# Kernel tuning notes

Hardware: AMD Instinct MI355X
Metric: run time of the kernel (lower is better)

## Reference

```python
import jax, jax.numpy as jnp
import numpy as np

N_NODES = 100_000
N_EDGES = 3_200_000


def setup_inputs() -> dict:
    key = jax.random.key(0)
    k = jax.random.split(key, 7)
    x = jax.random.normal(k[0], (N_NODES, 1), dtype=jnp.float32)
    edge_index = jax.random.randint(k[1], (2, N_EDGES), 0, N_NODES, dtype=jnp.int64)
    edge_weight = jax.random.uniform(k[2], (N_EDGES,), dtype=jnp.float32)
    # GCNConv params (glorot-style scale)
    W1 = jax.random.normal(k[3], (1, 16), dtype=jnp.float32) * 0.5
    b1 = jnp.zeros((16,), dtype=jnp.float32)
    W2 = jax.random.normal(k[4], (16, 2), dtype=jnp.float32) * 0.25
    b2 = jnp.zeros((2,), dtype=jnp.float32)
    return {"x": x, "edge_index": edge_index, "edge_weight": edge_weight,
            "W1": W1, "b1": b1, "W2": W2, "b2": b2}


def reference(x, edge_index, edge_weight, W1, b1, W2, b2):
    N = x.shape[0]
    src, dst = edge_index[0], edge_index[1]
    # GCN normalization with self-loops (fill value 1.0), cached across both layers
    loop = jnp.arange(N, dtype=edge_index.dtype)
    src_f = jnp.concatenate([src, loop])            # [E+N]
    dst_f = jnp.concatenate([dst, loop])            # [E+N]
    w_f = jnp.concatenate([edge_weight, jnp.ones((N,), dtype=edge_weight.dtype)])
    deg = jax.ops.segment_sum(w_f, dst_f, num_segments=N)   # [N]
    dinv = jnp.where(deg > 0, jax.lax.rsqrt(deg), 0.0)
    norm = dinv[src_f] * w_f * dinv[dst_f]          # [E+N]

    def gcn_layer(h, W, b):
        h = h @ W                                   # [N, F_out]
        msg = norm[:, None] * h[src_f]              # gather + weight  [E+N, F_out]
        agg = jax.ops.segment_sum(msg, dst_f, num_segments=N)  # scatter-add [N, F_out]
        return agg + b

    h = jax.nn.relu(gcn_layer(x, W1, b1))
    # F.dropout(training=self.training): identity at inference (reference is eval mode)
    out = gcn_layer(h, W2, b2)
    return jax.nn.log_softmax(out, axis=1)
```

## Files before the change

### kernel.cpp

```cpp
#include <hip/hip_runtime.h>
#include <math.h>


static constexpr int BS        = 512;
static constexpr int CHUNK     = 256;
static constexpr int LOG_CHUNK = 8;
static constexpr int MAXNB     = 512;
static constexpr int EPT_H     = 8192;
static constexpr int EPT_P     = 16384;


__global__ __launch_bounds__(BS) void zero_cnt_kernel(unsigned int* __restrict__ cnt,
                                                      int nb) {
    int t = threadIdx.x;
    if (t < nb) cnt[t] = 0u;
}

__global__ __launch_bounds__(BS) void hist_kernel(const int* __restrict__ dst,
                                                  unsigned int* __restrict__ cnt,
                                                  int E, int nb) {
    __shared__ unsigned int h[MAXNB];
    const int t = threadIdx.x;
    for (int i = t; i < nb; i += BS) h[i] = 0u;
    __syncthreads();
    const int base = blockIdx.x * EPT_H;
    const int nE   = min(EPT_H, E - base);
    for (int k = t; k < nE; k += BS)
        atomicAdd(&h[(unsigned int)dst[base + k] >> LOG_CHUNK], 1u);
    __syncthreads();
    for (int i = t; i < nb; i += BS) {
        unsigned int c = h[i];
        if (c) atomicAdd(&cnt[i], c);
    }
}

__global__ __launch_bounds__(BS) void scan_kernel(const unsigned int* __restrict__ cnt,
                                                  unsigned int* __restrict__ start,
                                                  unsigned int* __restrict__ cursor,
                                                  int nb) {
    __shared__ unsigned int s[MAXNB];
    const int t = threadIdx.x;
    unsigned int c = (t < nb) ? cnt[t] : 0u;
    s[t] = c;
    __syncthreads();
    for (int off = 1; off < MAXNB; off <<= 1) {
        unsigned int v = (t >= off) ? s[t - off] : 0u;
        __syncthreads();
        s[t] += v;
        __syncthreads();
    }
    if (t < nb) { start[t + 1] = s[t]; cursor[t] = s[t] - c; }
    if (t == 0) start[0] = 0u;
}

__global__ __launch_bounds__(BS) void place_kernel(
    const int* __restrict__ src, const int* __restrict__ dst,
    const float* __restrict__ w,
    unsigned int* __restrict__ cursor,
    unsigned long long* __restrict__ payload,
    int E, int nb) {
    __shared__ unsigned int h[MAXNB];
    __shared__ unsigned int lcur[MAXNB];
    const int base = blockIdx.x * EPT_P;
    const int nE   = min(EPT_P, E - base);
    const int t    = threadIdx.x;
    for (int i = t; i < nb; i += BS) h[i] = 0u;
    __syncthreads();
    int dc[EPT_P / BS];
    int cnt_ = 0;
    for (int k = t; k < nE; k += BS) {
        int d = dst[base + k];
        dc[cnt_++] = d;
        atomicAdd(&h[(unsigned int)d >> LOG_CHUNK], 1u);
    }
    __syncthreads();
    for (int i = t; i < nb; i += BS) {
        unsigned int c = h[i];
        lcur[i] = c ? atomicAdd(&cursor[i], c) : 0u;
    }
    __syncthreads();
    cnt_ = 0;
    for (int k = t; k < nE; k += BS) {
        int e = base + k;
        int d = dc[cnt_++];
        int b = (unsigned int)d >> LOG_CHUNK;
        unsigned int slot = atomicAdd(&lcur[b], 1u);
        unsigned long long p =
            ((unsigned long long)__float_as_uint(w[e]) << 32) |
            ((unsigned int)src[e] << LOG_CHUNK) |
            (unsigned int)(d & (CHUNK - 1));
        payload[slot] = p;
    }
}


__global__ __launch_bounds__(BS) void deg_dinv_kernel(
    const unsigned long long* __restrict__ payload,
    const unsigned int* __restrict__ start,
    const float* __restrict__ x,
    float* __restrict__ dinv, float* __restrict__ xd, int N) {
    __shared__ float acc[CHUNK];
    const int b = blockIdx.x, t = threadIdx.x;
    if (t < CHUNK) acc[t] = 0.0f;
    __syncthreads();
    const unsigned int s0 = start[b], s1 = start[b + 1];
    for (unsigned int i = s0 + t; i < s1; i += BS) {
        unsigned long long p = payload[i];
        atomicAdd(&acc[(unsigned int)p & (CHUNK - 1)],
                  __uint_as_float((unsigned int)(p >> 32)));
    }
    __syncthreads();
    int n = b * CHUNK + t;
    if (t < CHUNK && n < N) {
        float d = acc[t] + 1.0f;
        float r = (d > 0.0f) ? rsqrtf(d) : 0.0f;
        dinv[n] = r;
        xd[n]   = r * x[n];
    }
}

__global__ __launch_bounds__(BS) void s_gamma_kernel(
    const unsigned long long* __restrict__ payload,
    const unsigned int* __restrict__ start,
    const float* __restrict__ dinv,
    const float* __restrict__ xd,
    const float* __restrict__ W1,
    const float* __restrict__ b1,
    const float* __restrict__ W2,
    float* __restrict__ gd, int N) {
    __shared__ float acc[CHUNK];
    const int b = blockIdx.x, t = threadIdx.x;
    if (t < CHUNK) acc[t] = 0.0f;
    __syncthreads();
    const unsigned int s0 = start[b], s1 = start[b + 1];
    for (unsigned int i = s0 + t; i < s1; i += BS) {
        unsigned long long p = payload[i];
        float wv = __uint_as_float((unsigned int)(p >> 32));
        unsigned int lo32 = (unsigned int)p;
        atomicAdd(&acc[lo32 & (CHUNK - 1)], wv * xd[lo32 >> LOG_CHUNK]);
    }
    __syncthreads();
    int n = b * CHUNK + t;
    if (t < CHUNK && n < N) {
        float dv = dinv[n];
        float sv = dv * (acc[t] + xd[n]);
        float g = 0.0f;
#pragma unroll
        for (int f = 0; f < 16; ++f) {
            float h = fmaxf(sv * W1[f] + b1[f], 0.0f);
            g += h * (W2[2 * f + 1] - W2[2 * f + 0]);
        }
        gd[n] = dv * g;
    }
}

__global__ __launch_bounds__(BS) void d_out_kernel(
    const unsigned long long* __restrict__ payload,
    const unsigned int* __restrict__ start,
    const float* __restrict__ dinv,
    const float* __restrict__ gd,
    const float* __restrict__ b2,
    float* __restrict__ out, int N) {
    __shared__ float acc[CHUNK];
    const int b = blockIdx.x, t = threadIdx.x;
    if (t < CHUNK) acc[t] = 0.0f;
    __syncthreads();
    const unsigned int s0 = start[b], s1 = start[b + 1];
    for (unsigned int i = s0 + t; i < s1; i += BS) {
        unsigned long long p = payload[i];
        float wv = __uint_as_float((unsigned int)(p >> 32));
        unsigned int lo32 = (unsigned int)p;
        atomicAdd(&acc[lo32 & (CHUNK - 1)], wv * gd[lo32 >> LOG_CHUNK]);
    }
    __syncthreads();
    int n = b * CHUNK + t;
    if (t < CHUNK && n < N) {
        float dv = dinv[n];
        float d = dv * (acc[t] + gd[n]) + (b2[1] - b2[0]);
        float lse = fmaxf(d, 0.0f) + log1pf(expf(-fabsf(d)));
        out[2 * n + 0] = -lse;
        out[2 * n + 1] = d - lse;
    }
}


static constexpr int BLOCK = 256;

__global__ void zero_kernel(float* __restrict__ a, float* __restrict__ b, int n2) {
    int i = blockIdx.x * blockDim.x + threadIdx.x;
    if (i < n2) { a[i] = 0.0f; b[i] = 0.0f; }
}
__global__ void deg_kernel(const int* __restrict__ dst, const float* __restrict__ w,
                           float* __restrict__ deg, int E) {
    int e = blockIdx.x * blockDim.x + threadIdx.x;
    if (e < E) atomicAdd(&deg[dst[e]], w[e]);
}
__global__ void dinv_kernel(float* __restrict__ deg, int N) {
    int n = blockIdx.x * blockDim.x + threadIdx.x;
    if (n < N) {
        float d = deg[n] + 1.0f;
        deg[n] = (d > 0.0f) ? rsqrtf(d) : 0.0f;
    }
}
__global__ void s_kernel(const int* __restrict__ src, const int* __restrict__ dst,
                         const float* __restrict__ w, const float* __restrict__ dinv,
                         const float* __restrict__ x, float* __restrict__ s, int E) {
    int e = blockIdx.x * blockDim.x + threadIdx.x;
    if (e < E) {
        int si = src[e], di = dst[e];
        atomicAdd(&s[di], dinv[si] * w[e] * dinv[di] * x[si]);
    }
}
__global__ void g_kernel(const float* __restrict__ s, const float* __restrict__ dinv,
                         const float* __restrict__ x, const float* __restrict__ W1,
                         const float* __restrict__ b1, const float* __restrict__ W2,
                         float2* __restrict__ g, int N) {
    int n = blockIdx.x * blockDim.x + threadIdx.x;
    if (n < N) {
        float dv = dinv[n];
        float sv = s[n] + dv * dv * x[n];
        float g0 = 0.0f, g1 = 0.0f;
#pragma unroll
        for (int f = 0; f < 16; ++f) {
            float h = fmaxf(sv * W1[f] + b1[f], 0.0f);
            g0 += h * W2[2 * f + 0];
            g1 += h * W2[2 * f + 1];
        }
        g[n] = make_float2(g0, g1);
    }
}
__global__ void agg2_kernel(const int* __restrict__ src, const int* __restrict__ dst,
                            const float* __restrict__ w, const float* __restrict__ dinv,
                            const float2* __restrict__ g, float* __restrict__ agg, int E) {
    int e = blockIdx.x * blockDim.x + threadIdx.x;
    if (e < E) {
        int si = src[e], di = dst[e];
        float norm = dinv[si] * w[e] * dinv[di];
        float2 gv = g[si];
        atomicAdd(&agg[2 * di + 0], norm * gv.x);
        atomicAdd(&agg[2 * di + 1], norm * gv.y);
    }
}
__global__ void out_kernel(float* __restrict__ out, const float* __restrict__ dinv,
                           const float2* __restrict__ g, const float* __restrict__ b2, int N) {
    int n = blockIdx.x * blockDim.x + threadIdx.x;
    if (n < N) {
        float dv2 = dinv[n] * dinv[n];
        float2 gv = g[n];
        float a0 = out[2 * n + 0] + dv2 * gv.x + b2[0];
        float a1 = out[2 * n + 1] + dv2 * gv.y + b2[1];
        float m = fmaxf(a0, a1);
        float lse = m + logf(expf(a0 - m) + expf(a1 - m));
        out[2 * n + 0] = a0 - lse;
        out[2 * n + 1] = a1 - lse;
    }
}


extern "C" void kernel_launch(void* const* d_in, const int* in_sizes, int n_in,
                              void* d_out, int out_size, void* d_ws, size_t ws_size,
                              hipStream_t stream) {
    const float* x  = (const float*)d_in[0];
    const int*   ei = (const int*)d_in[1];
    const float* w  = (const float*)d_in[2];
    const float* W1 = (const float*)d_in[3];
    const float* b1 = (const float*)d_in[4];
    const float* W2 = (const float*)d_in[5];
    const float* b2 = (const float*)d_in[6];
    float* out = (float*)d_out;

    const int N = in_sizes[0];
    const int E = in_sizes[2];
    const int* src = ei;
    const int* dst = ei + E;

    const int nb = (N + CHUNK - 1) / CHUNK;

    size_t off = 0;
    size_t payload_off = off;  off += (size_t)E * 8;
    size_t cnt_off     = off;  off += (size_t)nb * 4;
    size_t start_off   = off;  off += (size_t)(nb + 1) * 4;
    size_t cursor_off  = off;  off += (size_t)nb * 4;
    off = (off + 7) & ~(size_t)7;
    size_t dinv_off    = off;  off += (size_t)N * 4;
    size_t xd_off      = off;  off += (size_t)N * 4;
    size_t gd_off      = off;  off += (size_t)N * 4;
    const size_t required = off;

    if (nb <= MAXNB && ws_size >= required) {
        char* wsb = (char*)d_ws;
        unsigned long long* payload = (unsigned long long*)(wsb + payload_off);
        unsigned int* cnt    = (unsigned int*)(wsb + cnt_off);
        unsigned int* startp = (unsigned int*)(wsb + start_off);
        unsigned int* cursor = (unsigned int*)(wsb + cursor_off);
        float* dinv = (float*)(wsb + dinv_off);
        float* xd   = (float*)(wsb + xd_off);
        float* gd   = (float*)(wsb + gd_off);

        const int gridH = (E + EPT_H - 1) / EPT_H;
        const int gridP = (E + EPT_P - 1) / EPT_P;

        zero_cnt_kernel<<<1,     BS, 0, stream>>>(cnt, nb);
        hist_kernel    <<<gridH, BS, 0, stream>>>(dst, cnt, E, nb);
        scan_kernel    <<<1,     BS, 0, stream>>>(cnt, startp, cursor, nb);
        place_kernel   <<<gridP, BS, 0, stream>>>(src, dst, w, cursor, payload, E, nb);
        deg_dinv_kernel<<<nb,    BS, 0, stream>>>(payload, startp, x, dinv, xd, N);
        s_gamma_kernel <<<nb,    BS, 0, stream>>>(payload, startp, dinv, xd, W1, b1, W2, gd, N);
        d_out_kernel   <<<nb,    BS, 0, stream>>>(payload, startp, dinv, gd, b2, out, N);
    } else {
        float*  ws   = (float*)d_ws;
        float*  dinv = ws;
        float*  s    = ws + (size_t)N;
        float2* g    = (float2*)(ws + (size_t)2 * N);
        const int gridE  = (E + BLOCK - 1) / BLOCK;
        const int gridN  = (N + BLOCK - 1) / BLOCK;
        const int gridN2 = (2 * N + BLOCK - 1) / BLOCK;
        zero_kernel<<<gridN2, BLOCK, 0, stream>>>(ws, out, 2 * N);
        deg_kernel <<<gridE,  BLOCK, 0, stream>>>(dst, w, dinv, E);
        dinv_kernel<<<gridN,  BLOCK, 0, stream>>>(dinv, N);
        s_kernel   <<<gridE,  BLOCK, 0, stream>>>(src, dst, w, dinv, x, s, E);
        g_kernel   <<<gridN,  BLOCK, 0, stream>>>(s, dinv, x, W1, b1, W2, g, N);
        agg2_kernel<<<gridE,  BLOCK, 0, stream>>>(src, dst, w, dinv, g, out, E);
        out_kernel <<<gridN,  BLOCK, 0, stream>>>(out, dinv, g, b2, N);
    }
}
```

Before: 211.1 us.

## Split edge payload into packed weight/dst and src arrays, vectorize CSR build

Replaces the 64-bit per-edge payload with two 32-bit arrays. One packs the edge weight, with its low 8 mantissa bits dropped, together with the local destination index; the other holds the source index. The degree pass now reads only 4 bytes per edge. Histogram and placement use int4/float4 loads with a unified 8192-edge tile, and the three aggregation kernels use 1024-thread blocks with a 4-way unrolled loop so more gathers are in flight. The cost is a small loss of weight precision and scattered writes into two arrays instead of one.

Result: slower. 223.8 us (+6.0%).

```diff
diff --git a/kernel.cpp b/kernel.cpp
--- a/kernel.cpp
+++ b/kernel.cpp
@@ -3,11 +3,11 @@
 
 
 static constexpr int BS        = 512;
+static constexpr int BSA       = 1024;
 static constexpr int CHUNK     = 256;
 static constexpr int LOG_CHUNK = 8;
 static constexpr int MAXNB     = 512;
-static constexpr int EPT_H     = 8192;
-static constexpr int EPT_P     = 16384;
+static constexpr int EPT       = 8192;
 
 
 __global__ __launch_bounds__(BS) void zero_cnt_kernel(unsigned int* __restrict__ cnt,
@@ -23,10 +23,22 @@
     const int t = threadIdx.x;
     for (int i = t; i < nb; i += BS) h[i] = 0u;
     __syncthreads();
-    const int base = blockIdx.x * EPT_H;
-    const int nE   = min(EPT_H, E - base);
-    for (int k = t; k < nE; k += BS)
-        atomicAdd(&h[(unsigned int)dst[base + k] >> LOG_CHUNK], 1u);
+    const int base = blockIdx.x * EPT;
+    const int nE   = min(EPT, E - base);
+    if (nE == EPT) {
+        const int4* d4 = (const int4*)(dst + base);
+#pragma unroll
+        for (int j = 0; j < EPT / (BS * 4); ++j) {
+            int4 v = d4[t + j * BS];
+            atomicAdd(&h[(unsigned int)v.x >> LOG_CHUNK], 1u);
+            atomicAdd(&h[(unsigned int)v.y >> LOG_CHUNK], 1u);
+            atomicAdd(&h[(unsigned int)v.z >> LOG_CHUNK], 1u);
+            atomicAdd(&h[(unsigned int)v.w >> LOG_CHUNK], 1u);
+        }
+    } else {
+        for (int k = t; k < nE; k += BS)
+            atomicAdd(&h[(unsigned int)dst[base + k] >> LOG_CHUNK], 1u);
+    }
     __syncthreads();
     for (int i = t; i < nb; i += BS) {
         unsigned int c = h[i];
@@ -57,21 +69,36 @@
     const int* __restrict__ src, const int* __restrict__ dst,
     const float* __restrict__ w,
     unsigned int* __restrict__ cursor,
-    unsigned long long* __restrict__ payload,
+    unsigned int* __restrict__ wq,
+    unsigned int* __restrict__ sr,
     int E, int nb) {
     __shared__ unsigned int h[MAXNB];
     __shared__ unsigned int lcur[MAXNB];
-    const int base = blockIdx.x * EPT_P;
-    const int nE   = min(EPT_P, E - base);
+    const int base = blockIdx.x * EPT;
+    const int nE   = min(EPT, E - base);
     const int t    = threadIdx.x;
     for (int i = t; i < nb; i += BS) h[i] = 0u;
     __syncthreads();
-    int dc[EPT_P / BS];
-    int cnt_ = 0;
-    for (int k = t; k < nE; k += BS) {
-        int d = dst[base + k];
-        dc[cnt_++] = d;
-        atomicAdd(&h[(unsigned int)d >> LOG_CHUNK], 1u);
+    int dreg[EPT / BS];
+    if (nE == EPT) {
+        const int4* d4 = (const int4*)(dst + base);
+#pragma unroll
+        for (int j = 0; j < EPT / (BS * 4); ++j) {
+            int4 v = d4[t + j * BS];
+            dreg[4 * j + 0] = v.x; dreg[4 * j + 1] = v.y;
+            dreg[4 * j + 2] = v.z; dreg[4 * j + 3] = v.w;
+            atomicAdd(&h[(unsigned int)v.x >> LOG_CHUNK], 1u);
+            atomicAdd(&h[(unsigned int)v.y >> LOG_CHUNK], 1u);
+            atomicAdd(&h[(unsigned int)v.z >> LOG_CHUNK], 1u);
+            atomicAdd(&h[(unsigned int)v.w >> LOG_CHUNK], 1u);
+        }
+    } else {
+        int c = 0;
+        for (int k = t; k < nE; k += BS) {
+            int d = dst[base + k];
+            dreg[c++] = d;
+            atomicAdd(&h[(unsigned int)d >> LOG_CHUNK], 1u);
+        }
     }
     __syncthreads();
     for (int i = t; i < nb; i += BS) {
@@ -79,23 +106,42 @@
         lcur[i] = c ? atomicAdd(&cursor[i], c) : 0u;
     }
     __syncthreads();
-    cnt_ = 0;
-    for (int k = t; k < nE; k += BS) {
-        int e = base + k;
-        int d = dc[cnt_++];
-        int b = (unsigned int)d >> LOG_CHUNK;
-        unsigned int slot = atomicAdd(&lcur[b], 1u);
-        unsigned long long p =
-            ((unsigned long long)__float_as_uint(w[e]) << 32) |
-            ((unsigned int)src[e] << LOG_CHUNK) |
-            (unsigned int)(d & (CHUNK - 1));
-        payload[slot] = p;
-    }
-}
-
-
-__global__ __launch_bounds__(BS) void deg_dinv_kernel(
-    const unsigned long long* __restrict__ payload,
+    if (nE == EPT) {
+        const int4*   s4 = (const int4*)(src + base);
+        const float4* w4 = (const float4*)(w + base);
+#pragma unroll
+        for (int j = 0; j < EPT / (BS * 4); ++j) {
+            int4   sv = s4[t + j * BS];
+            float4 wv = w4[t + j * BS];
+            int dd; unsigned int slot;
+#define PLACE_ONE(M, WF, SF)                                              \
+            dd   = dreg[4 * j + M];                                       \
+            slot = atomicAdd(&lcur[(unsigned int)dd >> LOG_CHUNK], 1u);   \
+            wq[slot] = (__float_as_uint(WF) & 0xFFFFFF00u) |              \
+                       (unsigned int)(dd & (CHUNK - 1));                  \
+            sr[slot] = (unsigned int)(SF);
+            PLACE_ONE(0, wv.x, sv.x)
+            PLACE_ONE(1, wv.y, sv.y)
+            PLACE_ONE(2, wv.z, sv.z)
+            PLACE_ONE(3, wv.w, sv.w)
+#undef PLACE_ONE
+        }
+    } else {
+        int c = 0;
+        for (int k = t; k < nE; k += BS) {
+            int e = base + k;
+            int dd = dreg[c++];
+            unsigned int slot = atomicAdd(&lcur[(unsigned int)dd >> LOG_CHUNK], 1u);
+            wq[slot] = (__float_as_uint(w[e]) & 0xFFFFFF00u) |
+                       (unsigned int)(dd & (CHUNK - 1));
+            sr[slot] = (unsigned int)src[e];
+        }
+    }
+}
+
+
+__global__ __launch_bounds__(BSA) void deg_dinv_kernel(
+    const unsigned int* __restrict__ wq,
     const unsigned int* __restrict__ start,
     const float* __restrict__ x,
     float* __restrict__ dinv, float* __restrict__ xd, int N) {
@@ -104,10 +150,17 @@
     if (t < CHUNK) acc[t] = 0.0f;
     __syncthreads();
     const unsigned int s0 = start[b], s1 = start[b + 1];
-    for (unsigned int i = s0 + t; i < s1; i += BS) {
-        unsigned long long p = payload[i];
-        atomicAdd(&acc[(unsigned int)p & (CHUNK - 1)],
-                  __uint_as_float((unsigned int)(p >> 32)));
+    unsigned int i = s0 + t;
+    for (; i + 3u * BSA < s1; i += 4u * BSA) {
+        unsigned int q0 = wq[i], q1 = wq[i + BSA], q2 = wq[i + 2 * BSA], q3 = wq[i + 3 * BSA];
+        atomicAdd(&acc[q0 & (CHUNK - 1)], __uint_as_float(q0 & 0xFFFFFF00u));
+        atomicAdd(&acc[q1 & (CHUNK - 1)], __uint_as_float(q1 & 0xFFFFFF00u));
+        atomicAdd(&acc[q2 & (CHUNK - 1)], __uint_as_float(q2 & 0xFFFFFF00u));
+        atomicAdd(&acc[q3 & (CHUNK - 1)], __uint_as_float(q3 & 0xFFFFFF00u));
+    }
+    for (; i < s1; i += BSA) {
+        unsigned int q = wq[i];
+        atomicAdd(&acc[q & (CHUNK - 1)], __uint_as_float(q & 0xFFFFFF00u));
     }
     __syncthreads();
     int n = b * CHUNK + t;
@@ -119,8 +172,9 @@
     }
 }
 
-__global__ __launch_bounds__(BS) void s_gamma_kernel(
-    const unsigned long long* __restrict__ payload,
+__global__ __launch_bounds__(BSA) void s_gamma_kernel(
+    const unsigned int* __restrict__ wq,
+    const unsigned int* __restrict__ sr,
     const unsigned int* __restrict__ start,
     const float* __restrict__ dinv,
     const float* __restrict__ xd,
@@ -133,11 +187,19 @@
     if (t < CHUNK) acc[t] = 0.0f;
     __syncthreads();
     const unsigned int s0 = start[b], s1 = start[b + 1];
-    for (unsigned int i = s0 + t; i < s1; i += BS) {
-        unsigned long long p = payload[i];
-        float wv = __uint_as_float((unsigned int)(p >> 32));
-        unsigned int lo32 = (unsigned int)p;
-        atomicAdd(&acc[lo32 & (CHUNK - 1)], wv * xd[lo32 >> LOG_CHUNK]);
+    unsigned int i = s0 + t;
+    for (; i + 3u * BSA < s1; i += 4u * BSA) {
+        unsigned int q0 = wq[i], q1 = wq[i + BSA], q2 = wq[i + 2 * BSA], q3 = wq[i + 3 * BSA];
+        unsigned int r0 = sr[i], r1 = sr[i + BSA], r2 = sr[i + 2 * BSA], r3 = sr[i + 3 * BSA];
+        float x0 = xd[r0], x1 = xd[r1], x2 = xd[r2], x3 = xd[r3];
+        atomicAdd(&acc[q0 & (CHUNK - 1)], __uint_as_float(q0 & 0xFFFFFF00u) * x0);
+        atomicAdd(&acc[q1 & (CHUNK - 1)], __uint_as_float(q1 & 0xFFFFFF00u) * x1);
+        atomicAdd(&acc[q2 & (CHUNK - 1)], __uint_as_float(q2 & 0xFFFFFF00u) * x2);
+        atomicAdd(&acc[q3 & (CHUNK - 1)], __uint_as_float(q3 & 0xFFFFFF00u) * x3);
+    }
+    for (; i < s1; i += BSA) {
+        unsigned int q = wq[i];
+        atomicAdd(&acc[q & (CHUNK - 1)], __uint_as_float(q & 0xFFFFFF00u) * xd[sr[i]]);
     }
     __syncthreads();
     int n = b * CHUNK + t;
@@ -154,8 +216,9 @@
     }
 }
 
-__global__ __launch_bounds__(BS) void d_out_kernel(
-    const unsigned long long* __restrict__ payload,
+__global__ __launch_bounds__(BSA) void d_out_kernel(
+    const unsigned int* __restrict__ wq,
+    const unsigned int* __restrict__ sr,
     const unsigned int* __restrict__ start,
     const float* __restrict__ dinv,
     const float* __restrict__ gd,
@@ -166,11 +229,19 @@
     if (t < CHUNK) acc[t] = 0.0f;
     __syncthreads();
     const unsigned int s0 = start[b], s1 = start[b + 1];
-    for (unsigned int i = s0 + t; i < s1; i += BS) {
-        unsigned long long p = payload[i];
-        float wv = __uint_as_float((unsigned int)(p >> 32));
-        unsigned int lo32 = (unsigned int)p;
-        atomicAdd(&acc[lo32 & (CHUNK - 1)], wv * gd[lo32 >> LOG_CHUNK]);
+    unsigned int i = s0 + t;
+    for (; i + 3u * BSA < s1; i += 4u * BSA) {
+        unsigned int q0 = wq[i], q1 = wq[i + BSA], q2 = wq[i + 2 * BSA], q3 = wq[i + 3 * BSA];
+        unsigned int r0 = sr[i], r1 = sr[i + BSA], r2 = sr[i + 2 * BSA], r3 = sr[i + 3 * BSA];
+        float g0 = gd[r0], g1 = gd[r1], g2 = gd[r2], g3 = gd[r3];
+        atomicAdd(&acc[q0 & (CHUNK - 1)], __uint_as_float(q0 & 0xFFFFFF00u) * g0);
+        atomicAdd(&acc[q1 & (CHUNK - 1)], __uint_as_float(q1 & 0xFFFFFF00u) * g1);
+        atomicAdd(&acc[q2 & (CHUNK - 1)], __uint_as_float(q2 & 0xFFFFFF00u) * g2);
+        atomicAdd(&acc[q3 & (CHUNK - 1)], __uint_as_float(q3 & 0xFFFFFF00u) * g3);
+    }
+    for (; i < s1; i += BSA) {
+        unsigned int q = wq[i];
+        atomicAdd(&acc[q & (CHUNK - 1)], __uint_as_float(q & 0xFFFFFF00u) * gd[sr[i]]);
     }
     __syncthreads();
     int n = b * CHUNK + t;
@@ -277,19 +348,20 @@
     const int nb = (N + CHUNK - 1) / CHUNK;
 
     size_t off = 0;
-    size_t payload_off = off;  off += (size_t)E * 8;
-    size_t cnt_off     = off;  off += (size_t)nb * 4;
-    size_t start_off   = off;  off += (size_t)(nb + 1) * 4;
-    size_t cursor_off  = off;  off += (size_t)nb * 4;
-    off = (off + 7) & ~(size_t)7;
-    size_t dinv_off    = off;  off += (size_t)N * 4;
-    size_t xd_off      = off;  off += (size_t)N * 4;
-    size_t gd_off      = off;  off += (size_t)N * 4;
+    size_t wq_off     = off;  off += (size_t)E * 4;
+    size_t sr_off     = off;  off += (size_t)E * 4;
+    size_t cnt_off    = off;  off += (size_t)nb * 4;
+    size_t start_off  = off;  off += (size_t)(nb + 1) * 4;
+    size_t cursor_off = off;  off += (size_t)nb * 4;
+    size_t dinv_off   = off;  off += (size_t)N * 4;
+    size_t xd_off     = off;  off += (size_t)N * 4;
+    size_t gd_off     = off;  off += (size_t)N * 4;
     const size_t required = off;
 
     if (nb <= MAXNB && ws_size >= required) {
         char* wsb = (char*)d_ws;
-        unsigned long long* payload = (unsigned long long*)(wsb + payload_off);
+        unsigned int* wq     = (unsigned int*)(wsb + wq_off);
+        unsigned int* sr     = (unsigned int*)(wsb + sr_off);
         unsigned int* cnt    = (unsigned int*)(wsb + cnt_off);
         unsigned int* startp = (unsigned int*)(wsb + start_off);
         unsigned int* cursor = (unsigned int*)(wsb + cursor_off);
@@ -297,16 +369,15 @@
         float* xd   = (float*)(wsb + xd_off);
         float* gd   = (float*)(wsb + gd_off);
 
-        const int gridH = (E + EPT_H - 1) / EPT_H;
-        const int gridP = (E + EPT_P - 1) / EPT_P;
-
-        zero_cnt_kernel<<<1,     BS, 0, stream>>>(cnt, nb);
-        hist_kernel    <<<gridH, BS, 0, stream>>>(dst, cnt, E, nb);
-        scan_kernel    <<<1,     BS, 0, stream>>>(cnt, startp, cursor, nb);
-        place_kernel   <<<gridP, BS, 0, stream>>>(src, dst, w, cursor, payload, E, nb);
-        deg_dinv_kernel<<<nb,    BS, 0, stream>>>(payload, startp, x, dinv, xd, N);
-        s_gamma_kernel <<<nb,    BS, 0, stream>>>(payload, startp, dinv, xd, W1, b1, W2, gd, N);
-        d_out_kernel   <<<nb,    BS, 0, stream>>>(payload, startp, dinv, gd, b2, out, N);
+        const int gridT = (E + EPT - 1) / EPT;
+
+        zero_cnt_kernel<<<1,     BS,  0, stream>>>(cnt, nb);
+        hist_kernel    <<<gridT, BS,  0, stream>>>(dst, cnt, E, nb);
+        scan_kernel    <<<1,     BS,  0, stream>>>(cnt, startp, cursor, nb);
+        place_kernel   <<<gridT, BS,  0, stream>>>(src, dst, w, cursor, wq, sr, E, nb);
+        deg_dinv_kernel<<<nb,    BSA, 0, stream>>>(wq, startp, x, dinv, xd, N);
+        s_gamma_kernel <<<nb,    BSA, 0, stream>>>(wq, sr, startp, dinv, xd, W1, b1, W2, gd, N);
+        d_out_kernel   <<<nb,    BSA, 0, stream>>>(wq, sr, startp, dinv, gd, b2, out, N);
     } else {
         float*  ws   = (float*)d_ws;
         float*  dinv = ws;
```

## Replace global bucket sort with per-tile local sort and split-K partial aggregation

Applied to the files above, without the earlier changes.

Drops the global histogram/scan/atomic-cursor pipeline. Each tile of edges is now sorted locally in shared memory into 4096-node buckets and writes per-tile row offsets. The three aggregation passes become split-K kernels: each block accumulates one bucket across a strided subset of tiles into a 4096-entry shared accumulator. Separate merge kernels then sum the K partials per node. This removes three launches and global atomics, and makes payload writes tile-contiguous. In exchange it adds partial-buffer traffic and three extra merge launches, and it reads many small, scattered per-tile segments.

Result: no change. 210.9 us (-0.1%).

```diff
diff --git a/kernel.cpp b/kernel.cpp
--- a/kernel.cpp
+++ b/kernel.cpp
@@ -2,185 +2,224 @@
 #include <math.h>
 
 
-static constexpr int BS        = 512;
-static constexpr int CHUNK     = 256;
-static constexpr int LOG_CHUNK = 8;
-static constexpr int MAXNB     = 512;
-static constexpr int EPT_H     = 8192;
-static constexpr int EPT_P     = 16384;
-
-
-__global__ __launch_bounds__(BS) void zero_cnt_kernel(unsigned int* __restrict__ cnt,
-                                                      int nb) {
-    int t = threadIdx.x;
-    if (t < nb) cnt[t] = 0u;
-}
-
-__global__ __launch_bounds__(BS) void hist_kernel(const int* __restrict__ dst,
-                                                  unsigned int* __restrict__ cnt,
-                                                  int E, int nb) {
-    __shared__ unsigned int h[MAXNB];
-    const int t = threadIdx.x;
-    for (int i = t; i < nb; i += BS) h[i] = 0u;
-    __syncthreads();
-    const int base = blockIdx.x * EPT_H;
-    const int nE   = min(EPT_H, E - base);
-    for (int k = t; k < nE; k += BS)
-        atomicAdd(&h[(unsigned int)dst[base + k] >> LOG_CHUNK], 1u);
-    __syncthreads();
-    for (int i = t; i < nb; i += BS) {
-        unsigned int c = h[i];
-        if (c) atomicAdd(&cnt[i], c);
-    }
-}
-
-__global__ __launch_bounds__(BS) void scan_kernel(const unsigned int* __restrict__ cnt,
-                                                  unsigned int* __restrict__ start,
-                                                  unsigned int* __restrict__ cursor,
-                                                  int nb) {
-    __shared__ unsigned int s[MAXNB];
-    const int t = threadIdx.x;
-    unsigned int c = (t < nb) ? cnt[t] : 0u;
-    s[t] = c;
-    __syncthreads();
-    for (int off = 1; off < MAXNB; off <<= 1) {
-        unsigned int v = (t >= off) ? s[t - off] : 0u;
-        __syncthreads();
-        s[t] += v;
-        __syncthreads();
-    }
-    if (t < nb) { start[t + 1] = s[t]; cursor[t] = s[t] - c; }
-    if (t == 0) start[0] = 0u;
-}
-
-__global__ __launch_bounds__(BS) void place_kernel(
+static constexpr int EPT    = 12288;
+static constexpr int BS_P   = 512;
+static constexpr int DREG   = EPT / BS_P;
+static constexpr int CHUNK  = 4096;
+static constexpr int LOGC   = 12;
+static constexpr int MAXNB  = 32;
+static constexpr int HREP   = 16;
+static constexpr int K      = 24;
+static constexpr int BSA    = 512;
+static constexpr int BSM    = 256;
+
+
+__global__ __launch_bounds__(BS_P) void place_kernel(
     const int* __restrict__ src, const int* __restrict__ dst,
     const float* __restrict__ w,
-    unsigned int* __restrict__ cursor,
+    unsigned int* __restrict__ rowOff,
     unsigned long long* __restrict__ payload,
     int E, int nb) {
-    __shared__ unsigned int h[MAXNB];
-    __shared__ unsigned int lcur[MAXNB];
-    const int base = blockIdx.x * EPT_P;
-    const int nE   = min(EPT_P, E - base);
+    __shared__ unsigned int perm[EPT];
+    __shared__ unsigned int h[HREP * 33];
+    __shared__ unsigned int cur[MAXNB + 1];
+    __shared__ unsigned int off[MAXNB + 1];
+    const int tile = blockIdx.x;
+    const int base = tile * EPT;
+    const int nE   = min(EPT, E - base);
     const int t    = threadIdx.x;
-    for (int i = t; i < nb; i += BS) h[i] = 0u;
-    __syncthreads();
-    int dc[EPT_P / BS];
-    int cnt_ = 0;
-    for (int k = t; k < nE; k += BS) {
-        int d = dst[base + k];
-        dc[cnt_++] = d;
-        atomicAdd(&h[(unsigned int)d >> LOG_CHUNK], 1u);
-    }
-    __syncthreads();
-    for (int i = t; i < nb; i += BS) {
-        unsigned int c = h[i];
-        lcur[i] = c ? atomicAdd(&cursor[i], c) : 0u;
-    }
-    __syncthreads();
-    cnt_ = 0;
-    for (int k = t; k < nE; k += BS) {
-        int e = base + k;
-        int d = dc[cnt_++];
-        int b = (unsigned int)d >> LOG_CHUNK;
-        unsigned int slot = atomicAdd(&lcur[b], 1u);
-        unsigned long long p =
-            ((unsigned long long)__float_as_uint(w[e]) << 32) |
-            ((unsigned int)src[e] << LOG_CHUNK) |
-            (unsigned int)(d & (CHUNK - 1));
-        payload[slot] = p;
-    }
-}
-
-
-__global__ __launch_bounds__(BS) void deg_dinv_kernel(
+
+    for (int i = t; i < HREP * 33; i += BS_P) h[i] = 0u;
+    __syncthreads();
+
+    int dreg[DREG];
+    {
+        int c = 0;
+        for (int k = t; k < nE; k += BS_P) {
+            int d = dst[base + k];
+            dreg[c++] = d;
+            atomicAdd(&h[(t & (HREP - 1)) * 33 + ((unsigned int)d >> LOGC)], 1u);
+        }
+    }
+    __syncthreads();
+    if (t < nb) {
+        unsigned int s = 0;
+#pragma unroll
+        for (int r = 0; r < HREP; ++r) s += h[r * 33 + t];
+        cur[t] = s;
+    }
+    __syncthreads();
+    if (t == 0) {
+        unsigned int run = 0;
+        for (int b = 0; b < nb; ++b) {
+            unsigned int c = cur[b];
+            off[b] = run; cur[b] = run; run += c;
+        }
+        off[nb] = run;
+    }
+    __syncthreads();
+    if (t <= nb) rowOff[(size_t)tile * (nb + 1) + t] = off[t];
+    {
+        int c = 0;
+        for (int k = t; k < nE; k += BS_P) {
+            int d = dreg[c++];
+            unsigned int slot = atomicAdd(&cur[(unsigned int)d >> LOGC], 1u);
+            perm[slot] = ((unsigned int)k << LOGC) | (unsigned int)(d & (CHUNK - 1));
+        }
+    }
+    __syncthreads();
+    for (int k = t; k < nE; k += BS_P) {
+        unsigned int pe = perm[k];
+        int j = (int)(pe >> LOGC);
+        unsigned int sv = (unsigned int)src[base + j];
+        float wv = w[base + j];
+        payload[(size_t)base + k] =
+            ((unsigned long long)__float_as_uint(wv) << 32) |
+            (sv << LOGC) | (pe & (CHUNK - 1));
+    }
+}
+
+
+__global__ __launch_bounds__(BSA) void deg_part_kernel(
     const unsigned long long* __restrict__ payload,
-    const unsigned int* __restrict__ start,
+    const unsigned int* __restrict__ rowOff,
+    float* __restrict__ partial,
+    int E, int nb, int nT) {
+    __shared__ float acc[CHUNK];
+    const int b = blockIdx.x / K, k = blockIdx.x % K;
+    const int t = threadIdx.x;
+    for (int i = t; i < CHUNK; i += BSA) acc[i] = 0.0f;
+    __syncthreads();
+    for (int tile = k; tile < nT; tile += K) {
+        unsigned int o0 = rowOff[(size_t)tile * (nb + 1) + b];
+        unsigned int o1 = rowOff[(size_t)tile * (nb + 1) + b + 1];
+        const unsigned long long* p = payload + (size_t)tile * EPT;
+        for (unsigned int i = o0 + t; i < o1; i += BSA) {
+            unsigned long long pv = p[i];
+            atomicAdd(&acc[(unsigned int)pv & (CHUNK - 1)],
+                      __uint_as_float((unsigned int)(pv >> 32)));
+        }
+    }
+    __syncthreads();
+    float* dp = partial + (size_t)blockIdx.x * CHUNK;
+    for (int i = t; i < CHUNK; i += BSA) dp[i] = acc[i];
+}
+
+__global__ __launch_bounds__(BSM) void deg_merge_kernel(
+    const float* __restrict__ partial,
     const float* __restrict__ x,
     float* __restrict__ dinv, float* __restrict__ xd, int N) {
+    int n = blockIdx.x * BSM + threadIdx.x;
+    if (n >= N) return;
+    int b = n >> LOGC, lo = n & (CHUNK - 1);
+    const float* pp = partial + ((size_t)b * K) * CHUNK + lo;
+    float s = 0.0f;
+#pragma unroll
+    for (int k = 0; k < K; ++k) s += pp[(size_t)k * CHUNK];
+    float d = s + 1.0f;
+    float r = (d > 0.0f) ? rsqrtf(d) : 0.0f;
+    dinv[n] = r;
+    xd[n]   = r * x[n];
+}
+
+__global__ __launch_bounds__(BSA) void s_part_kernel(
+    const unsigned long long* __restrict__ payload,
+    const unsigned int* __restrict__ rowOff,
+    const float* __restrict__ xd,
+    float* __restrict__ partial, int E, int nb, int nT) {
     __shared__ float acc[CHUNK];
-    const int b = blockIdx.x, t = threadIdx.x;
-    if (t < CHUNK) acc[t] = 0.0f;
-    __syncthreads();
-    const unsigned int s0 = start[b], s1 = start[b + 1];
-    for (unsigned int i = s0 + t; i < s1; i += BS) {
-        unsigned long long p = payload[i];
-        atomicAdd(&acc[(unsigned int)p & (CHUNK - 1)],
-                  __uint_as_float((unsigned int)(p >> 32)));
-    }
-    __syncthreads();
-    int n = b * CHUNK + t;
-    if (t < CHUNK && n < N) {
-        float d = acc[t] + 1.0f;
-        float r = (d > 0.0f) ? rsqrtf(d) : 0.0f;
-        dinv[n] = r;
-        xd[n]   = r * x[n];
-    }
-}
-
-__global__ __launch_bounds__(BS) void s_gamma_kernel(
-    const unsigned long long* __restrict__ payload,
-    const unsigned int* __restrict__ start,
+    const int b = blockIdx.x / K, k = blockIdx.x % K;
+    const int t = threadIdx.x;
+    for (int i = t; i < CHUNK; i += BSA) acc[i] = 0.0f;
+    __syncthreads();
+    for (int tile = k; tile < nT; tile += K) {
+        unsigned int o0 = rowOff[(size_t)tile * (nb + 1) + b];
+        unsigned int o1 = rowOff[(size_t)tile * (nb + 1) + b + 1];
+        const unsigned long long* p = payload + (size_t)tile * EPT;
+        for (unsigned int i = o0 + t; i < o1; i += BSA) {
+            unsigned long long pv = p[i];
+            unsigned int lo32 = (unsigned int)pv;
+            float xv = xd[(lo32 >> LOGC) & 0x1FFFFu];
+            atomicAdd(&acc[lo32 & (CHUNK - 1)],
+                      __uint_as_float((unsigned int)(pv >> 32)) * xv);
+        }
+    }
+    __syncthreads();
+    float* dp = partial + (size_t)blockIdx.x * CHUNK;
+    for (int i = t; i < CHUNK; i += BSA) dp[i] = acc[i];
+}
+
+__global__ __launch_bounds__(BSM) void s_merge_kernel(
+    const float* __restrict__ partial,
     const float* __restrict__ dinv,
     const float* __restrict__ xd,
     const float* __restrict__ W1,
     const float* __restrict__ b1,
     const float* __restrict__ W2,
     float* __restrict__ gd, int N) {
+    int n = blockIdx.x * BSM + threadIdx.x;
+    if (n >= N) return;
+    int b = n >> LOGC, lo = n & (CHUNK - 1);
+    const float* pp = partial + ((size_t)b * K) * CHUNK + lo;
+    float s = 0.0f;
+#pragma unroll
+    for (int k = 0; k < K; ++k) s += pp[(size_t)k * CHUNK];
+    float dv = dinv[n];
+    float sv = dv * (s + xd[n]);
+    float g = 0.0f;
+#pragma unroll
+    for (int f = 0; f < 16; ++f) {
+        float h = fmaxf(sv * W1[f] + b1[f], 0.0f);
+        g += h * (W2[2 * f + 1] - W2[2 * f + 0]);
+    }
+    gd[n] = dv * g;
+}
+
+__global__ __launch_bounds__(BSA) void d_part_kernel(
+    const unsigned long long* __restrict__ payload,
+    const unsigned int* __restrict__ rowOff,
+    const float* __restrict__ gd,
+    float* __restrict__ partial, int E, int nb, int nT) {
     __shared__ float acc[CHUNK];
-    const int b = blockIdx.x, t = threadIdx.x;
-    if (t < CHUNK) acc[t] = 0.0f;
-    __syncthreads();
-    const unsigned int s0 = start[b], s1 = start[b + 1];
-    for (unsigned int i = s0 + t; i < s1; i += BS) {
-        unsigned long long p = payload[i];
-        float wv = __uint_as_float((unsigned int)(p >> 32));
-        unsigned int lo32 = (unsigned int)p;
-        atomicAdd(&acc[lo32 & (CHUNK - 1)], wv * xd[lo32 >> LOG_CHUNK]);
-    }
-    __syncthreads();
-    int n = b * CHUNK + t;
-    if (t < CHUNK && n < N) {
-        float dv = dinv[n];
-        float sv = dv * (acc[t] + xd[n]);
-        float g = 0.0f;
-#pragma unroll
-        for (int f = 0; f < 16; ++f) {
-            float h = fmaxf(sv * W1[f] + b1[f], 0.0f);
-            g += h * (W2[2 * f + 1] - W2[2 * f + 0]);
-        }
-        gd[n] = dv * g;
-    }
-}
-
-__global__ __launch_bounds__(BS) void d_out_kernel(
-    const unsigned long long* __restrict__ payload,
-    const unsigned int* __restrict__ start,
+    const int b = blockIdx.x / K, k = blockIdx.x % K;
+    const int t = threadIdx.x;
+    for (int i = t; i < CHUNK; i += BSA) acc[i] = 0.0f;
+    __syncthreads();
+    for (int tile = k; tile < nT; tile += K) {
+        unsigned int o0 = rowOff[(size_t)tile * (nb + 1) + b];
+        unsigned int o1 = rowOff[(size_t)tile * (nb + 1) + b + 1];
+        const unsigned long long* p = payload + (size_t)tile * EPT;
+        for (unsigned int i = o0 + t; i < o1; i += BSA) {
+            unsigned long long pv = p[i];
+            unsigned int lo32 = (unsigned int)pv;
+            float gv = gd[(lo32 >> LOGC) & 0x1FFFFu];
+            atomicAdd(&acc[lo32 & (CHUNK - 1)],
+                      __uint_as_float((unsigned int)(pv >> 32)) * gv);
+        }
+    }
+    __syncthreads();
+    float* dp = partial + (size_t)blockIdx.x * CHUNK;
+    for (int i = t; i < CHUNK; i += BSA) dp[i] = acc[i];
+}
+
+__global__ __launch_bounds__(BSM) void d_merge_kernel(
+    const float* __restrict__ partial,
     const float* __restrict__ dinv,
     const float* __restrict__ gd,
     const float* __restrict__ b2,
     float* __restrict__ out, int N) {
-    __shared__ float acc[CHUNK];
-    const int b = blockIdx.x, t = threadIdx.x;
-    if (t < CHUNK) acc[t] = 0.0f;
-    __syncthreads();
-    const unsigned int s0 = start[b], s1 = start[b + 1];
-    for (unsigned int i = s0 + t; i < s1; i += BS) {
-        unsigned long long p = payload[i];
-        float wv = __uint_as_float((unsigned int)(p >> 32));
-        unsigned int lo32 = (unsigned int)p;
-        atomicAdd(&acc[lo32 & (CHUNK - 1)], wv * gd[lo32 >> LOG_CHUNK]);
-    }
-    __syncthreads();
-    int n = b * CHUNK + t;
-    if (t < CHUNK && n < N) {
-        float dv = dinv[n];
-        float d = dv * (acc[t] + gd[n]) + (b2[1] - b2[0]);
-        float lse = fmaxf(d, 0.0f) + log1pf(expf(-fabsf(d)));
-        out[2 * n + 0] = -lse;
-        out[2 * n + 1] = d - lse;
-    }
+    int n = blockIdx.x * BSM + threadIdx.x;
+    if (n >= N) return;
+    int b = n >> LOGC, lo = n & (CHUNK - 1);
+    const float* pp = partial + ((size_t)b * K) * CHUNK + lo;
+    float s = 0.0f;
+#pragma unroll
+    for (int k = 0; k < K; ++k) s += pp[(size_t)k * CHUNK];
+    float dv = dinv[n];
+    float d = dv * (s + gd[n]) + (b2[1] - b2[0]);
+    float lse = fmaxf(d, 0.0f) + log1pf(expf(-fabsf(d)));
+    out[2 * n + 0] = -lse;
+    out[2 * n + 1] = d - lse;
 }
 
 
@@ -275,38 +314,36 @@
     const int* dst = ei + E;
 
     const int nb = (N + CHUNK - 1) / CHUNK;
+    const int nT = (E + EPT - 1) / EPT;
 
     size_t off = 0;
-    size_t payload_off = off;  off += (size_t)E * 8;
-    size_t cnt_off     = off;  off += (size_t)nb * 4;
-    size_t start_off   = off;  off += (size_t)(nb + 1) * 4;
-    size_t cursor_off  = off;  off += (size_t)nb * 4;
+    size_t payload_off = off;  off += (size_t)nT * EPT * 8;
+    size_t rowoff_off  = off;  off += (size_t)nT * (nb + 1) * 4;
     off = (off + 7) & ~(size_t)7;
+    size_t partial_off = off;  off += (size_t)nb * K * CHUNK * 4;
     size_t dinv_off    = off;  off += (size_t)N * 4;
     size_t xd_off      = off;  off += (size_t)N * 4;
     size_t gd_off      = off;  off += (size_t)N * 4;
     const size_t required = off;
 
-    if (nb <= MAXNB && ws_size >= required) {
+    if (nb <= MAXNB && N <= 131072 && ws_size >= required) {
         char* wsb = (char*)d_ws;
         unsigned long long* payload = (unsigned long long*)(wsb + payload_off);
-        unsigned int* cnt    = (unsigned int*)(wsb + cnt_off);
-        unsigned int* startp = (unsigned int*)(wsb + start_off);
-        unsigned int* cursor = (unsigned int*)(wsb + cursor_off);
+        unsigned int* rowOff = (unsigned int*)(wsb + rowoff_off);
+        float* partial = (float*)(wsb + partial_off);
         float* dinv = (float*)(wsb + dinv_off);
         float* xd   = (float*)(wsb + xd_off);
         float* gd   = (float*)(wsb + gd_off);
 
-        const int gridH = (E + EPT_H - 1) / EPT_H;
-        const int gridP = (E + EPT_P - 1) / EPT_P;
-
-        zero_cnt_kernel<<<1,     BS, 0, stream>>>(cnt, nb);
-        hist_kernel    <<<gridH, BS, 0, stream>>>(dst, cnt, E, nb);
-        scan_kernel    <<<1,     BS, 0, stream>>>(cnt, startp, cursor, nb);
-        place_kernel   <<<gridP, BS, 0, stream>>>(src, dst, w, cursor, payload, E, nb);
-        deg_dinv_kernel<<<nb,    BS, 0, stream>>>(payload, startp, x, dinv, xd, N);
-        s_gamma_kernel <<<nb,    BS, 0, stream>>>(payload, startp, dinv, xd, W1, b1, W2, gd, N);
-        d_out_kernel   <<<nb,    BS, 0, stream>>>(payload, startp, dinv, gd, b2, out, N);
+        const int gridM = (N + BSM - 1) / BSM;
+
+        place_kernel    <<<nT,     BS_P, 0, stream>>>(src, dst, w, rowOff, payload, E, nb);
+        deg_part_kernel <<<nb * K, BSA,  0, stream>>>(payload, rowOff, partial, E, nb, nT);
+        deg_merge_kernel<<<gridM,  BSM,  0, stream>>>(partial, x, dinv, xd, N);
+        s_part_kernel   <<<nb * K, BSA,  0, stream>>>(payload, rowOff, xd, partial, E, nb, nT);
+        s_merge_kernel  <<<gridM,  BSM,  0, stream>>>(partial, dinv, xd, W1, b1, W2, gd, N);
+        d_part_kernel   <<<nb * K, BSA,  0, stream>>>(payload, rowOff, gd, partial, E, nb, nT);
+        d_merge_kernel  <<<gridM,  BSM,  0, stream>>>(partial, dinv, gd, b2, out, N);
     } else {
         float*  ws   = (float*)d_ws;
         float*  dinv = ws;
```
